# Optimization experiments

Hardware: AMD Instinct MI355X
Metric: run time of the kernel (lower is better)

Reference implementation:

```python
import jax, jax.numpy as jnp
import numpy as np

THRESH = 0.4


def setup_inputs() -> dict:
    key = jax.random.key(0)
    ks = jax.random.split(key, 8)
    B, N, C, H, O = 8, 16384, 640, 256, 128
    s = 0.02  # small init so sigmoid(logits) ~ 0.5 -> realistic mixed selection
    return {
        "point_features": jax.random.normal(ks[0], (B, N, C), jnp.float32),
        "point_coords": jax.random.normal(ks[1], (B, N, 3), jnp.float32) * 10.0,
        "w1": jax.random.normal(ks[2], (C, H), jnp.float32) * s,
        "b1": jnp.zeros((H,), jnp.float32),
        "w2": jax.random.normal(ks[3], (H, 1), jnp.float32) * s,
        "b2": jnp.zeros((1,), jnp.float32),
        "wo": jax.random.normal(ks[4], (C, O), jnp.float32) * s,
        "bo": jnp.zeros((O,), jnp.float32),
    }


def reference(point_features, point_coords, w1, b1, w2, b2, wo, bo):
    B, N, _ = point_features.shape
    # 2-layer MLP -> per-point logit -> sigmoid score
    h = jax.nn.relu(jnp.einsum('bnc,ch->bnh', point_features, w1) + b1)
    logits = jnp.einsum('bnh,ho->bno', h, w2) + b2          # [B, N, 1]
    scores = jax.nn.sigmoid(logits)                          # [B, N, 1]
    # score-scaled features through output projection
    feats = jnp.einsum('bnc,co->bno', point_features * scores, wo) + bo  # [B, N, O]
    # score-threshold selection + per-batch stream compaction into a
    # zero-padded tensor (padded to N, the jit-static worst case)
    sel = scores[..., 0] > THRESH                            # [B, N] bool
    pos = jnp.cumsum(sel.astype(jnp.int32), axis=1) - 1      # destination slot
    pos = jnp.where(sel, pos, N)                             # unselected -> OOB (dropped)
    bidx = jnp.arange(B)[:, None]
    selected_keypoints = jnp.zeros_like(feats).at[bidx, pos].set(feats, mode='drop')
    selected_coords = jnp.zeros_like(point_coords).at[bidx, pos].set(point_coords, mode='drop')
    # point_mask: True where the row is zero padding (matches (coords==0).sum(-1)!=0)
    point_mask = jnp.sum(selected_coords == 0, axis=-1) != 0
    return selected_keypoints, selected_coords, point_mask
```

## Files before the change

kernel.cpp:

```cpp
#include <hip/hip_runtime.h>
#include <hip/hip_bf16.h>


typedef __attribute__((ext_vector_type(8))) short short8v;
typedef __attribute__((ext_vector_type(4))) float f32x4;

#define M_TOTAL 131072
#define C_DIM 640
#define H_DIM 256
#define O_DIM 128
#define NCOMB 384
#define TM 64
#define KSTEPS 20
#define N_PTS 16384
#define TILES_PER_B 256
#define NTILES 2048
#define THRL -0.4054651081f
#define FIX_MARGIN 0.03f

#define OUT_COORD_OFF 16777216
#define OUT_MASK_OFF  17170432

#define WT_OFF     0u
#define TMASK_OFF  491520u
#define TAGG_OFF   507904u
#define TEXCL_OFF  516096u
#define COUNTS_OFF 524288u
#define G_OFF      1572864u

#define VMCNT(n) asm volatile("s_waitcnt vmcnt(" #n ")" ::: "memory")
#define LGKMCNT0 asm volatile("s_waitcnt lgkmcnt(0)" ::: "memory")
#define SBAR __builtin_amdgcn_s_barrier()
#define SCHED0 __builtin_amdgcn_sched_barrier(0)

__device__ __forceinline__ int swzB(int u) { return u ^ ((u >> 3) & 7); }

__device__ __forceinline__ void glds16(const void* g, void* l) {
  const __attribute__((address_space(1))) unsigned int* gp =
      reinterpret_cast<const __attribute__((address_space(1))) unsigned int*>(
          reinterpret_cast<uintptr_t>(g));
  __attribute__((address_space(3))) unsigned int* lp =
      reinterpret_cast<__attribute__((address_space(3))) unsigned int*>(
          reinterpret_cast<uintptr_t>(l));
  __builtin_amdgcn_global_load_lds(gp, lp, 16, 0, 0);
}

__device__ __forceinline__ unsigned int f2bf_bits(float f) {
  unsigned int u = __builtin_bit_cast(unsigned int, f);
  return (u + 0x7fffu + ((u >> 16) & 1u)) >> 16;
}
__device__ __forceinline__ unsigned int pack_bf2(float lo, float hi) {
  return f2bf_bits(lo) | (f2bf_bits(hi) << 16);
}

__global__ __launch_bounds__(256) void convert_w(const float* __restrict__ w1,
                                                 const float* __restrict__ wo,
                                                 unsigned short* __restrict__ Wt2) {
  int o = blockIdx.x * 256 + threadIdx.x;
  if (o < NCOMB * C_DIM) {
    int e = o & 7;
    int chunk = o >> 3;
    int ks = chunk / 1536;
    int r = chunk - ks * 1536;
    int u = swzB(r);
    int n = u >> 2, kg = u & 3;
    int k = ks * 32 + kg * 8 + e;
    float v = (n < H_DIM) ? w1[k * H_DIM + n] : wo[k * O_DIM + (n - H_DIM)];
    Wt2[o] = (unsigned short)f2bf_bits(v);
  }
}

__global__ __launch_bounds__(512, 4) void gemm_fused(
    const float* __restrict__ pf, const unsigned short* __restrict__ Wt2,
    const float* __restrict__ w1, const float* __restrict__ b1,
    const float* __restrict__ w2, const float* __restrict__ b2,
    const float* __restrict__ bo, unsigned long long* __restrict__ tmask,
    int* __restrict__ tagg, float* __restrict__ G) {
  __shared__ __align__(16) unsigned short As[2][2048];
  __shared__ __align__(16) unsigned short Bs[3][12288];

  const int tid = threadIdx.x;
  const int lane = tid & 63;
  const int wv = tid >> 6;
  const int q = lane & 15;
  const int p = lane >> 4;
  const int tile = blockIdx.x;
  const int m0 = tile * TM;

  f32x4 acc[3][4];
#pragma unroll
  for (int i = 0; i < 3; ++i)
#pragma unroll
    for (int rt = 0; rt < 4; ++rt) acc[i][rt] = (f32x4){0.f, 0.f, 0.f, 0.f};

  const float* asrc = pf + (size_t)(m0 + (tid >> 3)) * C_DIM + (tid & 7) * 4;
  const int aphys = ((tid >> 1) ^ ((tid >> 4) & 3)) * 8 + (tid & 1) * 4;
  const int aswz = (q >> 1) & 3;

  float4 Rcur, Rnext;
  {
    float4 R0 = *(const float4*)(asrc);
#pragma unroll
    for (int u = 0; u < 3; ++u)
      glds16(Wt2 + (size_t)(u * 512 + tid) * 8, &Bs[0][(u * 512 + tid) * 8]);
#pragma unroll
    for (int u = 0; u < 3; ++u)
      glds16(Wt2 + (size_t)(1536 + u * 512 + tid) * 8, &Bs[1][(u * 512 + tid) * 8]);
    Rcur = *(const float4*)(asrc + 32);
    *(uint2*)&As[0][aphys] = make_uint2(pack_bf2(R0.x, R0.y), pack_bf2(R0.z, R0.w));
    LGKMCNT0;
    VMCNT(4);
    SBAR;
  }

#pragma unroll
  for (int t = 0; t < KSTEPS; ++t) {
    short8v af01[2], af23[2], bf[3];
#pragma unroll
    for (int rt = 0; rt < 2; ++rt)
      af01[rt] = *(const short8v*)&As[t & 1][((rt * 64 + q * 4 + p) ^ aswz) * 8];
#pragma unroll
    for (int i = 0; i < 3; ++i) {
      const int ub = (((wv + 8 * i) * 16 + q) << 2) + p;
      bf[i] = *(const short8v*)&Bs[t % 3][swzB(ub) * 8];
    }
    if (t + 2 < KSTEPS) {
      Rnext = *(const float4*)(asrc + (t + 2) * 32);
#pragma unroll
      for (int u = 0; u < 3; ++u)
        glds16(Wt2 + (size_t)((t + 2) * 1536 + u * 512 + tid) * 8,
               &Bs[(t + 2) % 3][(u * 512 + tid) * 8]);
    }
    SBAR;
    LGKMCNT0;
    SCHED0;
    __builtin_amdgcn_s_setprio(1);
#pragma unroll
    for (int i = 0; i < 3; ++i)
#pragma unroll
      for (int rt = 0; rt < 2; ++rt)
        acc[i][rt] = __builtin_amdgcn_mfma_f32_16x16x32_bf16(af01[rt], bf[i],
                                                             acc[i][rt], 0, 0, 0);
    __builtin_amdgcn_s_setprio(0);
    SBAR;
#pragma unroll
    for (int rt = 2; rt < 4; ++rt)
      af23[rt - 2] = *(const short8v*)&As[t & 1][((rt * 64 + q * 4 + p) ^ aswz) * 8];
    if (t + 1 < KSTEPS) {
      *(uint2*)&As[(t + 1) & 1][aphys] =
          make_uint2(pack_bf2(Rcur.x, Rcur.y), pack_bf2(Rcur.z, Rcur.w));
      Rcur = Rnext;
    }
    LGKMCNT0;
    if (t + 2 < KSTEPS) { VMCNT(4); } else { VMCNT(0); }
    SBAR;
    SCHED0;
    __builtin_amdgcn_s_setprio(1);
#pragma unroll
    for (int i = 0; i < 3; ++i)
#pragma unroll
      for (int rt = 2; rt < 4; ++rt)
        acc[i][rt] = __builtin_amdgcn_mfma_f32_16x16x32_bf16(af23[rt - 2], bf[i],
                                                             acc[i][rt], 0, 0, 0);
    __builtin_amdgcn_s_setprio(0);
    SBAR;
  }
  __syncthreads();

  float* lpart = (float*)&As[0][0];
  float* llog = (float*)&Bs[0][0];
  float* srow = llog + 64;
  float* fsum = srow + 64;
  unsigned long long* s_fixmask = (unsigned long long*)(fsum + 4);

  float w2v[2], b1v[2];
#pragma unroll
  for (int i = 0; i < 2; ++i) {
    int col = (wv + 8 * i) * 16 + q;
    w2v[i] = w2[col];
    b1v[i] = b1[col];
  }
#pragma unroll
  for (int rt = 0; rt < 4; ++rt) {
    float pr[4] = {0.f, 0.f, 0.f, 0.f};
#pragma unroll
    for (int i = 0; i < 2; ++i)
#pragma unroll
      for (int r = 0; r < 4; ++r)
        pr[r] += fmaxf(acc[i][rt][r] + b1v[i], 0.f) * w2v[i];
#pragma unroll
    for (int mk = 1; mk < 16; mk <<= 1)
#pragma unroll
      for (int r = 0; r < 4; ++r) pr[r] += __shfl_xor(pr[r], mk);
    if (q == 0)
#pragma unroll
      for (int r = 0; r < 4; ++r) lpart[wv * 64 + rt * 16 + p * 4 + r] = pr[r];
  }
  __syncthreads();

  bool nf = false;
  if (wv == 0) {
    float lg = b2[0];
#pragma unroll
    for (int w = 0; w < 8; ++w) lg += lpart[w * 64 + tid];
    llog[tid] = lg;
    nf = fabsf(lg - THRL) < FIX_MARGIN;
  }
  unsigned long long fm = __ballot(nf);
  if (tid == 0) *s_fixmask = fm;
  __syncthreads();

  unsigned long long fixmask = *s_fixmask;
  while (fixmask) {
    int row = __ffsll(fixmask) - 1;
    fixmask &= fixmask - 1;
    if (tid < 256) {
      const float* prow = pf + (size_t)(m0 + row) * C_DIM;
      float a0 = 0.f, a1 = 0.f;
      for (int c = 0; c < C_DIM; c += 2) {
        a0 = fmaf(prow[c], w1[(size_t)c * H_DIM + tid], a0);
        a1 = fmaf(prow[c + 1], w1[(size_t)(c + 1) * H_DIM + tid], a1);
      }
      float v = fmaxf(a0 + a1 + b1[tid], 0.f) * w2[tid];
#pragma unroll
      for (int mk = 1; mk < 64; mk <<= 1) v += __shfl_xor(v, mk);
      if (lane == 0) fsum[wv] = v;
    }
    __syncthreads();
    if (tid == 0)
      llog[row] = fsum[0] + fsum[1] + fsum[2] + fsum[3] + b2[0];
    __syncthreads();
  }

  bool sel = false;
  float flog = 0.f;
  if (wv == 0) {
    flog = llog[tid];
    sel = flog > THRL;
  }
  unsigned long long selmask = __ballot(sel);
  if (wv == 0) {
    srow[tid] = 1.f / (1.f + expf(-flog));
    if (tid == 0) {
      tmask[tile] = selmask;
      tagg[tile] = __popcll(selmask);
    }
  }
  __syncthreads();

  {
    const int gcol = wv * 16 + q;
    const float bov = bo[gcol];
#pragma unroll
    for (int rt = 0; rt < 4; ++rt)
#pragma unroll
      for (int r = 0; r < 4; ++r) {
        int row = rt * 16 + p * 4 + r;
        G[(size_t)(m0 + row) * O_DIM + gcol] = fmaf(acc[2][rt][r], srow[row], bov);
      }
  }
}

__global__ __launch_bounds__(256) void scan_tiles(const int* __restrict__ tagg,
                                                  int* __restrict__ texcl,
                                                  int* __restrict__ counts) {
  __shared__ int wsum[4];
  const int c = blockIdx.x, t = threadIdx.x;
  const int lane = t & 63, w = t >> 6;
  int v = tagg[c * 256 + t];
  int inc = v;
#pragma unroll
  for (int d = 1; d < 64; d <<= 1) {
    int n = __shfl_up(inc, d);
    if (lane >= d) inc += n;
  }
  if (lane == 63) wsum[w] = inc;
  __syncthreads();
  int base = 0;
#pragma unroll
  for (int ww = 0; ww < 4; ++ww)
    if (ww < w) base += wsum[ww];
  texcl[c * 256 + t] = base + inc - v;
  if (t == 255) counts[c] = base + inc;
}

__global__ __launch_bounds__(512) void scatter(
    const float* __restrict__ G, const unsigned long long* __restrict__ tmask,
    const int* __restrict__ texcl, const float* __restrict__ pc,
    float* __restrict__ out) {
  const int tile = blockIdx.x;
  const int tid = threadIdx.x;
  const int lane = tid & 63;
  const int wv = tid >> 6;
  const unsigned long long mask = tmask[tile];
  const int base = (tile >> 8) * N_PTS + texcl[tile];
  const int m0 = tile * TM;
#pragma unroll
  for (int j = 0; j < 8; ++j) {
    const int row = wv * 8 + j;
    if (!((mask >> row) & 1ull)) continue;
    const int dst = base + __popcll(mask & ((1ull << row) - 1ull));
    const int m = m0 + row;
    float2 g = *(const float2*)(G + (size_t)m * O_DIM + lane * 2);
    *(float2*)(out + (size_t)dst * O_DIM + lane * 2) = g;
    if (lane == 0) {
      float c0 = pc[m * 3], c1 = pc[m * 3 + 1], c2 = pc[m * 3 + 2];
      float* oc = out + OUT_COORD_OFF;
      oc[dst * 3] = c0; oc[dst * 3 + 1] = c1; oc[dst * 3 + 2] = c2;
      out[OUT_MASK_OFF + dst] = (c0 == 0.f || c1 == 0.f || c2 == 0.f) ? 1.f : 0.f;
    }
  }
}

__global__ __launch_bounds__(256) void fill_tail(const int* __restrict__ counts,
                                                 float* __restrict__ out) {
  const int lane = threadIdx.x & 63;
  for (int m = blockIdx.x * 4 + (threadIdx.x >> 6); m < M_TOTAL; m += 8192) {
    int b = m >> 14, j = m & (N_PTS - 1);
    if (j < counts[b]) continue;
    *(float2*)(out + (size_t)m * O_DIM + lane * 2) = make_float2(0.f, 0.f);
    if (lane == 0) {
      float* oc = out + OUT_COORD_OFF;
      oc[m * 3] = 0.f; oc[m * 3 + 1] = 0.f; oc[m * 3 + 2] = 0.f;
      out[OUT_MASK_OFF + m] = 1.f;
    }
  }
}

extern "C" void kernel_launch(void* const* d_in, const int* in_sizes, int n_in,
                              void* d_out, int out_size, void* d_ws, size_t ws_size,
                              hipStream_t stream) {
  const float* pf = (const float*)d_in[0];
  const float* pc = (const float*)d_in[1];
  const float* w1 = (const float*)d_in[2];
  const float* b1 = (const float*)d_in[3];
  const float* w2 = (const float*)d_in[4];
  const float* b2 = (const float*)d_in[5];
  const float* wo = (const float*)d_in[6];
  const float* bo = (const float*)d_in[7];
  float* out = (float*)d_out;
  char* ws = (char*)d_ws;

  unsigned short* Wt2 = (unsigned short*)(ws + WT_OFF);
  unsigned long long* tmask = (unsigned long long*)(ws + TMASK_OFF);
  int* tagg = (int*)(ws + TAGG_OFF);
  int* texcl = (int*)(ws + TEXCL_OFF);
  int* counts = (int*)(ws + COUNTS_OFF);
  float* G = (float*)(ws + G_OFF);

  convert_w<<<960, 256, 0, stream>>>(w1, wo, Wt2);
  gemm_fused<<<NTILES, 512, 0, stream>>>(pf, Wt2, w1, b1, w2, b2, bo,
                                         tmask, tagg, G);
  scan_tiles<<<8, 256, 0, stream>>>(tagg, texcl, counts);
  scatter<<<NTILES, 512, 0, stream>>>(G, tmask, texcl, pc, out);
  fill_tail<<<2048, 256, 0, stream>>>(counts, out);
}
```

Measured before the change: 193.7 us.

## Load weight fragments straight into registers and drop LDS staging for B

The fused GEMM now reads the bf16 weight matrix directly from global memory into per-wave MFMA fragment registers, prefetched one K-step ahead. The conversion kernel writes the weights in a fragment-major layout so each lane's load is contiguous. The A tile moves to a triple buffer with a single barrier per K-step instead of two, and the LDS footprint shrinks to the A buffers only. This removes the LDS round trip and the extra barriers for B. In exchange, every wave depends on L2 latency for its weights with only one step of prefetch.

```diff
diff --git a/kernel.cpp b/kernel.cpp
--- a/kernel.cpp
+++ b/kernel.cpp
@@ -28,22 +28,9 @@
 #define COUNTS_OFF 524288u
 #define G_OFF      1572864u
 
-#define VMCNT(n) asm volatile("s_waitcnt vmcnt(" #n ")" ::: "memory")
 #define LGKMCNT0 asm volatile("s_waitcnt lgkmcnt(0)" ::: "memory")
 #define SBAR __builtin_amdgcn_s_barrier()
 #define SCHED0 __builtin_amdgcn_sched_barrier(0)
-
-__device__ __forceinline__ int swzB(int u) { return u ^ ((u >> 3) & 7); }
-
-__device__ __forceinline__ void glds16(const void* g, void* l) {
-  const __attribute__((address_space(1))) unsigned int* gp =
-      reinterpret_cast<const __attribute__((address_space(1))) unsigned int*>(
-          reinterpret_cast<uintptr_t>(g));
-  __attribute__((address_space(3))) unsigned int* lp =
-      reinterpret_cast<__attribute__((address_space(3))) unsigned int*>(
-          reinterpret_cast<uintptr_t>(l));
-  __builtin_amdgcn_global_load_lds(gp, lp, 16, 0, 0);
-}
 
 __device__ __forceinline__ unsigned int f2bf_bits(float f) {
   unsigned int u = __builtin_bit_cast(unsigned int, f);
@@ -59,12 +46,14 @@
   int o = blockIdx.x * 256 + threadIdx.x;
   if (o < NCOMB * C_DIM) {
     int e = o & 7;
-    int chunk = o >> 3;
-    int ks = chunk / 1536;
-    int r = chunk - ks * 1536;
-    int u = swzB(r);
-    int n = u >> 2, kg = u & 3;
-    int k = ks * 32 + kg * 8 + e;
+    int g = o >> 3;
+    int pp = g & 3;
+    int qq = (g >> 2) & 15;
+    int tc = g >> 6;
+    int ct = tc % 24;
+    int t = tc / 24;
+    int k = t * 32 + pp * 8 + e;
+    int n = ct * 16 + qq;
     float v = (n < H_DIM) ? w1[k * H_DIM + n] : wo[k * O_DIM + (n - H_DIM)];
     Wt2[o] = (unsigned short)f2bf_bits(v);
   }
@@ -76,8 +65,7 @@
     const float* __restrict__ w2, const float* __restrict__ b2,
     const float* __restrict__ bo, unsigned long long* __restrict__ tmask,
     int* __restrict__ tagg, float* __restrict__ G) {
-  __shared__ __align__(16) unsigned short As[2][2048];
-  __shared__ __align__(16) unsigned short Bs[3][12288];
+  __shared__ __align__(16) unsigned short As[3][2048];
 
   const int tid = threadIdx.x;
   const int lane = tid & 63;
@@ -97,78 +85,57 @@
   const int aphys = ((tid >> 1) ^ ((tid >> 4) & 3)) * 8 + (tid & 1) * 4;
   const int aswz = (q >> 1) & 3;
 
-  float4 Rcur, Rnext;
+  const unsigned short* bbase = Wt2 + wv * 512 + q * 32 + p * 8;
+
+  float4 Rcur;
+  short8v bc0, bc1, bc2;
   {
     float4 R0 = *(const float4*)(asrc);
-#pragma unroll
-    for (int u = 0; u < 3; ++u)
-      glds16(Wt2 + (size_t)(u * 512 + tid) * 8, &Bs[0][(u * 512 + tid) * 8]);
-#pragma unroll
-    for (int u = 0; u < 3; ++u)
-      glds16(Wt2 + (size_t)(1536 + u * 512 + tid) * 8, &Bs[1][(u * 512 + tid) * 8]);
+    bc0 = *(const short8v*)(bbase);
+    bc1 = *(const short8v*)(bbase + 4096);
+    bc2 = *(const short8v*)(bbase + 8192);
     Rcur = *(const float4*)(asrc + 32);
     *(uint2*)&As[0][aphys] = make_uint2(pack_bf2(R0.x, R0.y), pack_bf2(R0.z, R0.w));
     LGKMCNT0;
-    VMCNT(4);
+    SCHED0;
     SBAR;
   }
 
 #pragma unroll
   for (int t = 0; t < KSTEPS; ++t) {
-    short8v af01[2], af23[2], bf[3];
-#pragma unroll
-    for (int rt = 0; rt < 2; ++rt)
-      af01[rt] = *(const short8v*)&As[t & 1][((rt * 64 + q * 4 + p) ^ aswz) * 8];
-#pragma unroll
-    for (int i = 0; i < 3; ++i) {
-      const int ub = (((wv + 8 * i) * 16 + q) << 2) + p;
-      bf[i] = *(const short8v*)&Bs[t % 3][swzB(ub) * 8];
-    }
-    if (t + 2 < KSTEPS) {
-      Rnext = *(const float4*)(asrc + (t + 2) * 32);
-#pragma unroll
-      for (int u = 0; u < 3; ++u)
-        glds16(Wt2 + (size_t)((t + 2) * 1536 + u * 512 + tid) * 8,
-               &Bs[(t + 2) % 3][(u * 512 + tid) * 8]);
-    }
-    SBAR;
+    float4 Rnext;
+    short8v bn0, bn1, bn2;
+    if (t + 2 < KSTEPS) Rnext = *(const float4*)(asrc + (t + 2) * 32);
+    if (t + 1 < KSTEPS) {
+      const unsigned short* bp = bbase + (size_t)(t + 1) * 12288;
+      bn0 = *(const short8v*)(bp);
+      bn1 = *(const short8v*)(bp + 4096);
+      bn2 = *(const short8v*)(bp + 8192);
+      *(uint2*)&As[(t + 1) % 3][aphys] =
+          make_uint2(pack_bf2(Rcur.x, Rcur.y), pack_bf2(Rcur.z, Rcur.w));
+      Rcur = Rnext;
+    }
     LGKMCNT0;
     SCHED0;
+    SBAR;
+    short8v af[4];
+#pragma unroll
+    for (int rt = 0; rt < 4; ++rt)
+      af[rt] = *(const short8v*)&As[t % 3][((rt * 64 + q * 4 + p) ^ aswz) * 8];
     __builtin_amdgcn_s_setprio(1);
 #pragma unroll
-    for (int i = 0; i < 3; ++i)
-#pragma unroll
-      for (int rt = 0; rt < 2; ++rt)
-        acc[i][rt] = __builtin_amdgcn_mfma_f32_16x16x32_bf16(af01[rt], bf[i],
-                                                             acc[i][rt], 0, 0, 0);
+    for (int rt = 0; rt < 4; ++rt) {
+      acc[0][rt] = __builtin_amdgcn_mfma_f32_16x16x32_bf16(af[rt], bc0, acc[0][rt], 0, 0, 0);
+      acc[1][rt] = __builtin_amdgcn_mfma_f32_16x16x32_bf16(af[rt], bc1, acc[1][rt], 0, 0, 0);
+      acc[2][rt] = __builtin_amdgcn_mfma_f32_16x16x32_bf16(af[rt], bc2, acc[2][rt], 0, 0, 0);
+    }
     __builtin_amdgcn_s_setprio(0);
-    SBAR;
-#pragma unroll
-    for (int rt = 2; rt < 4; ++rt)
-      af23[rt - 2] = *(const short8v*)&As[t & 1][((rt * 64 + q * 4 + p) ^ aswz) * 8];
-    if (t + 1 < KSTEPS) {
-      *(uint2*)&As[(t + 1) & 1][aphys] =
-          make_uint2(pack_bf2(Rcur.x, Rcur.y), pack_bf2(Rcur.z, Rcur.w));
-      Rcur = Rnext;
-    }
-    LGKMCNT0;
-    if (t + 2 < KSTEPS) { VMCNT(4); } else { VMCNT(0); }
-    SBAR;
-    SCHED0;
-    __builtin_amdgcn_s_setprio(1);
-#pragma unroll
-    for (int i = 0; i < 3; ++i)
-#pragma unroll
-      for (int rt = 2; rt < 4; ++rt)
-        acc[i][rt] = __builtin_amdgcn_mfma_f32_16x16x32_bf16(af23[rt - 2], bf[i],
-                                                             acc[i][rt], 0, 0, 0);
-    __builtin_amdgcn_s_setprio(0);
-    SBAR;
+    bc0 = bn0; bc1 = bn1; bc2 = bn2;
   }
   __syncthreads();
 
   float* lpart = (float*)&As[0][0];
-  float* llog = (float*)&Bs[0][0];
+  float* llog = (float*)&As[1][0];
   float* srow = llog + 64;
   float* fsum = srow + 64;
   unsigned long long* s_fixmask = (unsigned long long*)(fsum + 4);
```

New measurement: 184.4 us. 4.8% less time.
